# Kernel optimization log

Measured on AMD Instinct MI355X. Metric: run time of the kernel, lower is better.

Reference implementation:

```python
import jax, jax.numpy as jnp
import numpy as np

N = 20000   # nodes
E = 160000  # edges
IN = 16     # in_channels
H = 32      # hidden_channels
MID = 32    # edge-MLP hidden width


def setup_inputs() -> dict:
    key = jax.random.key(0)
    ks = jax.random.split(key, 18)
    s = 0.1  # param scale
    return {
        "x": jax.random.normal(ks[0], (N, IN), jnp.float32),
        "edge_index": jax.random.randint(ks[1], (2, E), 0, N, dtype=jnp.int64),
        "edge_weight": jax.random.uniform(ks[2], (E,), jnp.float32),
        # edge_net1: Linear(1,32) -> SiLU -> Linear(32, IN*H)
        "en1_w1": jax.random.normal(ks[3], (1, MID), jnp.float32) * s,
        "en1_b1": jax.random.normal(ks[4], (MID,), jnp.float32) * s,
        "en1_w2": jax.random.normal(ks[5], (MID, IN * H), jnp.float32) * s,
        "en1_b2": jax.random.normal(ks[6], (IN * H,), jnp.float32) * s,
        "root1": jax.random.normal(ks[7], (IN, H), jnp.float32) * s,
        "bias1": jax.random.normal(ks[8], (H,), jnp.float32) * s,
        # edge_net2: Linear(1,32) -> SiLU -> Linear(32, H*H)
        "en2_w1": jax.random.normal(ks[9], (1, MID), jnp.float32) * s,
        "en2_b1": jax.random.normal(ks[10], (MID,), jnp.float32) * s,
        "en2_w2": jax.random.normal(ks[11], (MID, H * H), jnp.float32) * s,
        "en2_b2": jax.random.normal(ks[12], (H * H,), jnp.float32) * s,
        "root2": jax.random.normal(ks[13], (H, H), jnp.float32) * s,
        "bias2": jax.random.normal(ks[14], (H,), jnp.float32) * s,
        "dec_w": jax.random.normal(ks[15], (H, 1), jnp.float32) * s,
        "dec_b": jax.random.normal(ks[16], (1,), jnp.float32) * s,
    }


def _nnconv(x, src, dst, inv_cnt, e, w1, b1, w2, b2, root, bias, cin, cout):
    # edge MLP -> per-edge [cin, cout] weight matrix
    h = jax.nn.silu(e @ w1 + b1)            # [E, MID]
    w = (h @ w2 + b2).reshape(-1, cin, cout)  # [E, cin, cout]
    msg = jnp.einsum('ei,eio->eo', x[src], w)  # per-edge matmul [E, cout]
    agg = jax.ops.segment_sum(msg, dst, num_segments=N) * inv_cnt  # scatter-mean
    return agg + x @ root + bias


def reference(x, edge_index, edge_weight,
              en1_w1, en1_b1, en1_w2, en1_b2, root1, bias1,
              en2_w1, en2_b1, en2_w2, en2_b2, root2, bias2,
              dec_w, dec_b):
    src, dst = edge_index[0], edge_index[1]
    e = edge_weight[:, None]  # [E, 1]
    cnt = jax.ops.segment_sum(jnp.ones((E,), x.dtype), dst, num_segments=N)
    inv_cnt = (1.0 / jnp.maximum(cnt, 1.0))[:, None]  # [N, 1]
    h = _nnconv(x, src, dst, inv_cnt, e, en1_w1, en1_b1, en1_w2, en1_b2, root1, bias1, IN, H)
    h = jax.nn.silu(h)
    h = _nnconv(h, src, dst, inv_cnt, e, en2_w1, en2_b1, en2_w2, en2_b2, root2, bias2, H, H)
    h = jax.nn.silu(h)
    out = h @ dec_w + dec_b  # [N, 1]
    return out[:, 0]
```

## Files before the change

kernel.cpp:

```cpp
#include <hip/hip_runtime.h>
#include <hip/hip_bf16.h>

#define NN 20000
#define EE 160000
#define HH 32
#define MIDD 32
#define NB 64
#define EPB 2500

typedef _Float16 f16x4 __attribute__((ext_vector_type(4)));
typedef _Float16 f16x8 __attribute__((ext_vector_type(8)));
typedef float f32x4 __attribute__((ext_vector_type(4)));

__device__ __forceinline__ float silu_f(float v) {
    return __fdividef(v, 1.0f + __expf(-v));
}

__device__ __forceinline__ void gload_lds_b32(const void* gsrc, void* ldst) {
    __builtin_amdgcn_global_load_lds(
        (const __attribute__((address_space(1))) void*)gsrc,
        (__attribute__((address_space(3))) void*)ldst, 4, 0, 0);
}

__device__ __forceinline__ int swz4(int e) { return ((e >> 2) & 3) << 2; }

__global__ __launch_bounds__(256) void prep_kernel(
    const int* __restrict__ ei,
    const float* __restrict__ w2a, const float* __restrict__ b2a,
    const float* __restrict__ ra,
    const float* __restrict__ w2b, const float* __restrict__ b2b,
    const float* __restrict__ rb,
    const float* __restrict__ x,
    unsigned int* __restrict__ histG,
    _Float16* __restrict__ Wt1, _Float16* __restrict__ Wt2,
    _Float16* __restrict__ x16, int* __restrict__ flag) {
    const int t = threadIdx.x;
    if (blockIdx.x < NB) {
        __shared__ unsigned int h2[NN / 2];
        for (int i = t; i < NN / 2; i += 256) h2[i] = 0u;
        __syncthreads();
        const int base = blockIdx.x * EPB;
        for (int e = base + t; e < base + EPB; e += 256) {
            int d = ei[EE + e];
            atomicAdd(&h2[d >> 1], 1u << ((d & 1) * 16));
        }
        __syncthreads();
        unsigned int* outp = histG + (size_t)blockIdx.x * NN;
        for (int n = t; n < NN; n += 256)
            outp[n] = (h2[n >> 1] >> ((n & 1) * 16)) & 0xFFFFu;
        return;
    }
    if (blockIdx.x == NB && t == 0) *flag = 0;
    int idx = (blockIdx.x - NB) * 256 + t;
    if (idx < 17408) {
        int o = idx / 544, k = idx % 544;
        float v;
        if (k < 512) {
            int m = k & 31, i = k >> 5;
            v = w2a[m * 512 + i * 32 + o];
        } else if (k < 528) {
            v = b2a[(k - 512) * 32 + o];
        } else {
            v = ra[(k - 528) * 32 + o];
        }
        Wt1[o * 544 + k] = (_Float16)v;
    } else if (idx < 52224) {
        int j = idx - 17408;
        int o = j / 1088, k = j % 1088;
        float v;
        if (k < 1024) {
            int m = k & 31, i = k >> 5;
            v = w2b[m * 1024 + i * 32 + o];
        } else if (k < 1056) {
            v = b2b[(k - 1024) * 32 + o];
        } else {
            v = rb[(k - 1056) * 32 + o];
        }
        Wt2[o * 1088 + k] = (_Float16)v;
    } else if (idx < 52224 + NN * 16) {
        int j = idx - 52224;
        x16[j] = (_Float16)x[j];
    }
}

__global__ __launch_bounds__(256) void colscan_scan_kernel(
    unsigned int* __restrict__ histG, int* __restrict__ cnt,
    float* __restrict__ invc, int* __restrict__ off, int* __restrict__ flag) {
    const int n = blockIdx.x * 256 + threadIdx.x;
    if (n < NN) {
        unsigned int s = 0;
        #pragma unroll 4
        for (int b = 0; b < NB; ++b) {
            unsigned int v = histG[(size_t)b * NN + n];
            histG[(size_t)b * NN + n] = s;
            s += v;
        }
        cnt[n] = (int)s;
        invc[n] = 1.0f / fmaxf((float)s, 1.0f);
    }
    __threadfence();
    __shared__ int isLast;
    __shared__ int wtot[4];
    if (threadIdx.x == 0)
        isLast = (atomicAdd(flag, 1) == (int)gridDim.x - 1) ? 1 : 0;
    __syncthreads();
    if (!isLast) return;

    const int t = threadIdx.x;
    const int base = t * 80;
    int s = 0;
    if (base + 80 <= NN) {
        #pragma unroll
        for (int q = 0; q < 20; ++q) {
            int4 v = ((const int4*)(cnt + base))[q];
            s += v.x + v.y + v.z + v.w;
        }
    }
    const int lane = t & 63, wv = t >> 6;
    int incl = s;
    #pragma unroll
    for (int d2 = 1; d2 < 64; d2 <<= 1) {
        int u = __shfl_up(incl, d2);
        if (lane >= d2) incl += u;
    }
    if (lane == 63) wtot[wv] = incl;
    __syncthreads();
    int wbase = 0;
    for (int p2 = 0; p2 < wv; ++p2) wbase += wtot[p2];
    int running = wbase + incl - s;
    if (base + 80 <= NN) {
        #pragma unroll
        for (int q = 0; q < 20; ++q) {
            int4 v = ((const int4*)(cnt + base))[q];
            int4 o;
            o.x = running;
            o.y = running + v.x;
            o.z = o.y + v.y;
            o.w = o.z + v.z;
            ((int4*)(off + base))[q] = o;
            running = o.w + v.w;
        }
    }
    if (t == 0) off[NN] = EE;
}

__global__ __launch_bounds__(256) void scatter2_kernel(
    const int* __restrict__ ei, const float* __restrict__ ewt,
    const int* __restrict__ off, const unsigned int* __restrict__ histG,
    int2* __restrict__ spair) {
    __shared__ unsigned int r2[NN / 2];
    const int t = threadIdx.x, b = blockIdx.x;
    for (int i = t; i < NN / 2; i += 256) r2[i] = 0u;
    __syncthreads();
    const int base = b * EPB;
    const unsigned int* hb = histG + (size_t)b * NN;
    for (int e = base + t; e < base + EPB; e += 256) {
        int d = ei[EE + e];
        unsigned int old = atomicAdd(&r2[d >> 1], 1u << ((d & 1) * 16));
        int rank = (int)((old >> ((d & 1) * 16)) & 0xFFFFu);
        int pos = off[d] + (int)hb[d] + rank;
        spair[pos] = make_int2(ei[e], __float_as_int(ewt[e]));
    }
}


template <int CIN, bool DECODE>
__global__ __launch_bounds__(512, 4) void fused_layer(
    const _Float16* __restrict__ xin16, const int* __restrict__ spair,
    const int* __restrict__ off, const float* __restrict__ invc,
    const float* __restrict__ w1, const float* __restrict__ b1,
    const _Float16* __restrict__ Wt, const float* __restrict__ bias,
    void* __restrict__ outp, const float* __restrict__ dw,
    const float* __restrict__ db) {
    constexpr int K = 34 * CIN;
    constexpr int LDK = K + 4;
    constexpr int steps = K / 32;
    constexpr int CAP = 192;
    constexpr int RPG = 128 / CIN;
    constexpr int LPR = CIN / 2;
    constexpr int NIH = CIN / 16;

    extern __shared__ char smem[];
    _Float16* Fl = (_Float16*)smem;
    char* poolb = smem + (size_t)16 * LDK * 2;
    int* Ps = (int*)poolb;
    _Float16* Xs = (_Float16*)(poolb + (2 * CAP + 64) * 4);
    _Float16* Hs = Xs + CAP * CIN;
    float* red = (float*)poolb;

    const int t = threadIdx.x;
    const int n0 = blockIdx.x * 16;
    const int lane = t & 63, w = t >> 6;
    const int col = lane & 15, g4 = (lane >> 4) * 4;
    const int qcl = col & 1, qhi = col >> 1;

    const int E0 = off[n0], E1 = off[n0 + 16];
    const int L = E1 - E0;

    const int d0 = n0 + w * 2;
    const int e0l0 = off[d0] - E0;
    const int e1l0 = off[d0 + 1] - E0;
    const int e1l1 = off[d0 + 2] - E0;

    const float w1v = w1[t & 31];
    const float b1v = b1[t & 31];

    f32x4 aS[2][2][NIH];
    f32x4 a0[2][NIH];
    #pragma unroll
    for (int c = 0; c < 2; ++c) {
        #pragma unroll
        for (int mh = 0; mh < 2; ++mh)
            #pragma unroll
            for (int ih = 0; ih < NIH; ++ih) aS[c][mh][ih] = (f32x4){0.f, 0.f, 0.f, 0.f};
        #pragma unroll
        for (int ih = 0; ih < NIH; ++ih) a0[c][ih] = (f32x4){0.f, 0.f, 0.f, 0.f};
    }

    for (int base = 0; base < L; base += CAP) {
        const int Lc = (L - base < CAP) ? (L - base) : CAP;

        for (int c = w * 64; c < 2 * Lc; c += 512) {
            int gidx = 2 * (E0 + base) + c + lane;
            gidx = (gidx < 2 * EE) ? gidx : (2 * EE - 1);
            gload_lds_b32(spair + gidx, Ps + c);
        }
        __syncthreads();

        {
            const int G = (Lc + RPG - 1) / RPG;
            const int er = lane / LPR, ecp = lane % LPR;
            for (int p = w; p < G; p += 8) {
                int el = p * RPG + er; el = (el < Lc - 1) ? el : (Lc - 1);
                int sn = Ps[2 * el];
                int sp = (CIN == 32) ? (ecp ^ swz4(el)) : ecp;
                gload_lds_b32(xin16 + (size_t)sn * CIN + 2 * sp,
                              Xs + (size_t)p * RPG * CIN);
            }
        }
        for (int idx = t; idx < Lc * 32; idx += 512) {
            int e = idx >> 5, m = idx & 31;
            float ew = __int_as_float(Ps[2 * e + 1]);
            int slot = (((m >> 1) ^ swz4(e)) << 1) + (m & 1);
            Hs[e * 32 + slot] = (_Float16)silu_f(fmaf(ew, w1v, b1v));
        }
        __syncthreads();

        #pragma unroll
        for (int c = 0; c < 2; ++c) {
            int lo = ((c == 0) ? e0l0 : e1l0) - base;
            int hi = ((c == 0) ? e1l0 : e1l1) - base;
            lo = (lo < 0) ? 0 : lo;
            hi = (hi > Lc) ? Lc : hi;
            for (int ks = lo; ks < hi; ks += 32) {
                f16x8 bf[NIH];
                #pragma unroll
                for (int ih = 0; ih < NIH; ++ih) {
                    const int qx = ih * 8 + qhi;
                    #pragma unroll
                    for (int j = 0; j < 4; ++j) {
                        int k1 = ks + g4 + j, k2 = k1 + 16;
                        int c1 = (k1 < hi) ? k1 : (Lc - 1);
                        int c2 = (k2 < hi) ? k2 : (Lc - 1);
                        if (CIN == 32) {
                            bf[ih][j]     = Xs[c1 * 32 + ((qx ^ swz4(c1)) << 1) + qcl];
                            bf[ih][j + 4] = Xs[c2 * 32 + ((qx ^ swz4(c2)) << 1) + qcl];
                        } else {
                            bf[ih][j]     = Xs[c1 * CIN + ih * 16 + col];
                            bf[ih][j + 4] = Xs[c2 * CIN + ih * 16 + col];
                        }
                    }
                }
                f16x8 af[2];
                #pragma unroll
                for (int mh = 0; mh < 2; ++mh) {
                    const int qh = mh * 8 + qhi;
                    #pragma unroll
                    for (int j = 0; j < 4; ++j) {
                        int k1 = ks + g4 + j, k2 = k1 + 16;
                        int c1 = (k1 < hi) ? k1 : (Lc - 1);
                        int c2 = (k2 < hi) ? k2 : (Lc - 1);
                        _Float16 v1 = Hs[c1 * 32 + ((qh ^ swz4(c1)) << 1) + qcl];
                        _Float16 v2 = Hs[c2 * 32 + ((qh ^ swz4(c2)) << 1) + qcl];
                        af[mh][j]     = (k1 < hi) ? v1 : (_Float16)0;
                        af[mh][j + 4] = (k2 < hi) ? v2 : (_Float16)0;
                    }
                }
                f16x8 ao;
                #pragma unroll
                for (int j = 0; j < 4; ++j) {
                    int k1 = ks + g4 + j, k2 = k1 + 16;
                    ao[j]     = (col == 0 && k1 < hi) ? (_Float16)1 : (_Float16)0;
                    ao[j + 4] = (col == 0 && k2 < hi) ? (_Float16)1 : (_Float16)0;
                }
                #pragma unroll
                for (int mh = 0; mh < 2; ++mh)
                    #pragma unroll
                    for (int ih = 0; ih < NIH; ++ih)
                        aS[c][mh][ih] = __builtin_amdgcn_mfma_f32_16x16x32_f16(
                            af[mh], bf[ih], aS[c][mh][ih], 0, 0, 0);
                #pragma unroll
                for (int ih = 0; ih < NIH; ++ih)
                    a0[c][ih] = __builtin_amdgcn_mfma_f32_16x16x32_f16(
                        ao, bf[ih], a0[c][ih], 0, 0, 0);
            }
        }
        if (base + CAP < L) __syncthreads();
    }

    #pragma unroll
    for (int c = 0; c < 2; ++c) {
        const int d = n0 + w * 2 + c;
        const float iv = invc[d];
        _Float16* Fr = Fl + (size_t)(w * 2 + c) * LDK;
        #pragma unroll
        for (int mh = 0; mh < 2; ++mh)
            #pragma unroll
            for (int ih = 0; ih < NIH; ++ih)
                #pragma unroll
                for (int r = 0; r < 4; ++r)
                    Fr[32 * (ih * 16 + col) + mh * 16 + g4 + r] =
                        (_Float16)(aS[c][mh][ih][r] * iv);
        if (g4 == 0) {
            #pragma unroll
            for (int ih = 0; ih < NIH; ++ih)
                Fr[32 * CIN + ih * 16 + col] = (_Float16)(a0[c][ih][0] * iv);
        }
        if (lane >= CIN && lane < 2 * CIN)
            Fr[32 * CIN + lane] = xin16[(size_t)d * CIN + (lane - CIN)];
    }
    __syncthreads();

    const int o16 = col, g = lane >> 4;

    const _Float16* Arow = Fl + (size_t)o16 * LDK + g * 4;
    const _Float16* B0 = Wt + (size_t)o16 * K + g * 4;
    const _Float16* B1 = Wt + (size_t)(o16 + 16) * K + g * 4;

    f32x4 acc0 = {0.f, 0.f, 0.f, 0.f};
    f32x4 acc1 = {0.f, 0.f, 0.f, 0.f};

    const int sb = (steps * w) >> 3;
    const int se = (steps * (w + 1)) >> 3;
    #pragma unroll 2
    for (int s = sb; s < se; ++s) {
        const int k0 = s * 32;
        f16x4 alo = *(const f16x4*)(Arow + k0);
        f16x4 ahi = *(const f16x4*)(Arow + k0 + 16);
        f16x4 b0l = *(const f16x4*)(B0 + k0);
        f16x4 b0h = *(const f16x4*)(B0 + k0 + 16);
        f16x4 b1l = *(const f16x4*)(B1 + k0);
        f16x4 b1h = *(const f16x4*)(B1 + k0 + 16);
        f16x8 a, bb0, bb1;
        #pragma unroll
        for (int j = 0; j < 4; ++j) {
            a[j] = alo[j];  a[j + 4] = ahi[j];
            bb0[j] = b0l[j]; bb0[j + 4] = b0h[j];
            bb1[j] = b1l[j]; bb1[j + 4] = b1h[j];
        }
        acc0 = __builtin_amdgcn_mfma_f32_16x16x32_f16(a, bb0, acc0, 0, 0, 0);
        acc1 = __builtin_amdgcn_mfma_f32_16x16x32_f16(a, bb1, acc1, 0, 0, 0);
    }

    if (w > 0) {
        float* rw = red + (w - 1) * 512;
        #pragma unroll
        for (int r = 0; r < 4; ++r) {
            rw[(g * 4 + r) * 32 + o16]      = acc0[r];
            rw[(g * 4 + r) * 32 + 16 + o16] = acc1[r];
        }
    }
    __syncthreads();
    if (w == 0) {
        #pragma unroll
        for (int r = 0; r < 4; ++r) {
            const int ro = (g * 4 + r) * 32 + o16;
            #pragma unroll
            for (int p = 0; p < 7; ++p) {
                acc0[r] += red[p * 512 + ro];
                acc1[r] += red[p * 512 + ro + 16];
            }
        }
        const float bb0 = bias[o16], bb1 = bias[o16 + 16];
        const int nrow = n0 + g * 4;
        if (!DECODE) {
            _Float16* op = (_Float16*)outp;
            #pragma unroll
            for (int r = 0; r < 4; ++r) {
                op[(size_t)(nrow + r) * 32 + o16]      = (_Float16)silu_f(acc0[r] + bb0);
                op[(size_t)(nrow + r) * 32 + 16 + o16] = (_Float16)silu_f(acc1[r] + bb1);
            }
        } else {
            float* op = (float*)outp;
            const float w0 = dw[o16], w1vv = dw[o16 + 16];
            const float dbv = db[0];
            #pragma unroll
            for (int r = 0; r < 4; ++r) {
                float p = silu_f(acc0[r] + bb0) * w0 + silu_f(acc1[r] + bb1) * w1vv;
                p += __shfl_xor(p, 1);
                p += __shfl_xor(p, 2);
                p += __shfl_xor(p, 4);
                p += __shfl_xor(p, 8);
                if (o16 == 0) op[nrow + r] = p + dbv;
            }
        }
    }
}


extern "C" void kernel_launch(void* const* d_in, const int* in_sizes, int n_in,
                              void* d_out, int out_size, void* d_ws, size_t ws_size,
                              hipStream_t stream) {
    const float* x      = (const float*)d_in[0];
    const int*   ei     = (const int*)d_in[1];
    const float* ew     = (const float*)d_in[2];
    const float* en1_w1 = (const float*)d_in[3];
    const float* en1_b1 = (const float*)d_in[4];
    const float* en1_w2 = (const float*)d_in[5];
    const float* en1_b2 = (const float*)d_in[6];
    const float* root1  = (const float*)d_in[7];
    const float* bias1  = (const float*)d_in[8];
    const float* en2_w1 = (const float*)d_in[9];
    const float* en2_b1 = (const float*)d_in[10];
    const float* en2_w2 = (const float*)d_in[11];
    const float* en2_b2 = (const float*)d_in[12];
    const float* root2  = (const float*)d_in[13];
    const float* bias2  = (const float*)d_in[14];
    const float* dec_w  = (const float*)d_in[15];
    const float* dec_b  = (const float*)d_in[16];
    float* out = (float*)d_out;
    (void)in_sizes; (void)n_in; (void)out_size; (void)ws_size;

    char* wp = (char*)d_ws;
    auto alloc = [&](size_t bytes) {
        char* p = wp;
        wp += (bytes + 255) & ~(size_t)255;
        return p;
    };
    unsigned int* histG = (unsigned int*)alloc((size_t)NB * NN * 4);
    int*      cnt   = (int*)alloc((size_t)NN * 4);
    int*      off   = (int*)alloc((size_t)(NN + 1) * 4);
    float*    invc  = (float*)alloc((size_t)NN * 4);
    int2*     spair = (int2*)alloc((size_t)EE * 8);
    _Float16* h1h   = (_Float16*)alloc((size_t)NN * 32 * 2);
    _Float16* x16   = (_Float16*)alloc((size_t)NN * 16 * 2);
    _Float16* Wt1   = (_Float16*)alloc((size_t)17408 * 2);
    _Float16* Wt2   = (_Float16*)alloc((size_t)34816 * 2);
    int*      flag  = (int*)alloc(256);

    const int build_blocks = (52224 + NN * 16 + 255) / 256;
    prep_kernel<<<NB + build_blocks, 256, 0, stream>>>(
        ei, en1_w2, en1_b2, root1, en2_w2, en2_b2, root2, x,
        histG, Wt1, Wt2, x16, flag);
    colscan_scan_kernel<<<(NN + 255) / 256, 256, 0, stream>>>(
        histG, cnt, invc, off, flag);
    scatter2_kernel<<<NB, 256, 0, stream>>>(ei, ew, off, histG, spair);

    auto f1 = fused_layer<16, false>;
    auto f2 = fused_layer<32, true>;
    (void)hipFuncSetAttribute((const void*)f1,
                              hipFuncAttributeMaxDynamicSharedMemorySize, 163840);
    (void)hipFuncSetAttribute((const void*)f2,
                              hipFuncAttributeMaxDynamicSharedMemorySize, 163840);

    const size_t lds1 = (size_t)16 * (34 * 16 + 4) * 2 + (448 * 4 + 192 * 16 * 2 + 192 * 64);
    const size_t lds2 = (size_t)16 * (34 * 32 + 4) * 2 + (448 * 4 + 192 * 32 * 2 + 192 * 64);

    fused_layer<16, false><<<NN / 16, 512, lds1, stream>>>(
        x16, (const int*)spair, off, invc, en1_w1, en1_b1, Wt1, bias1, h1h,
        nullptr, nullptr);
    fused_layer<32, true><<<NN / 16, 512, lds2, stream>>>(
        h1h, (const int*)spair, off, invc, en2_w1, en2_b1, Wt2, bias2, out,
        dec_w, dec_b);
}
```

Baseline: 104.7 us.

## Drop LDS XOR swizzle, pad edge tiles, and double prep histogram blocks

Removes the XOR swizzle on the gathered X and H tiles in LDS and uses plain row-major indexing. The tiles get padding rows, and the gather loads 32 extra clamped rows, so the MFMA operand loads no longer need per-element index clamping and the address arithmetic gets simpler. Separately, the histogram/scatter stage now uses 128 blocks with half as many edges each instead of 64. Without the swizzle, the column-strided LDS reads may hit more bank conflicts, and the padded buffers raise LDS use per block.

```diff
diff --git a/kernel.cpp b/kernel.cpp
--- a/kernel.cpp
+++ b/kernel.cpp
@@ -5,8 +5,8 @@
 #define EE 160000
 #define HH 32
 #define MIDD 32
-#define NB 64
-#define EPB 2500
+#define NB 128
+#define EPB 1250
 
 typedef _Float16 f16x4 __attribute__((ext_vector_type(4)));
 typedef _Float16 f16x8 __attribute__((ext_vector_type(8)));
@@ -21,8 +21,6 @@
         (const __attribute__((address_space(1))) void*)gsrc,
         (__attribute__((address_space(3))) void*)ldst, 4, 0, 0);
 }
-
-__device__ __forceinline__ int swz4(int e) { return ((e >> 2) & 3) << 2; }
 
 __global__ __launch_bounds__(256) void prep_kernel(
     const int* __restrict__ ei,
@@ -179,20 +177,21 @@
     constexpr int RPG = 128 / CIN;
     constexpr int LPR = CIN / 2;
     constexpr int NIH = CIN / 16;
+    constexpr int XROWS = CAP + 40;
+    constexpr int HROWS = CAP + 32;
 
     extern __shared__ char smem[];
     _Float16* Fl = (_Float16*)smem;
     char* poolb = smem + (size_t)16 * LDK * 2;
     int* Ps = (int*)poolb;
     _Float16* Xs = (_Float16*)(poolb + (2 * CAP + 64) * 4);
-    _Float16* Hs = Xs + CAP * CIN;
+    _Float16* Hs = Xs + XROWS * CIN;
     float* red = (float*)poolb;
 
     const int t = threadIdx.x;
     const int n0 = blockIdx.x * 16;
     const int lane = t & 63, w = t >> 6;
     const int col = lane & 15, g4 = (lane >> 4) * 4;
-    const int qcl = col & 1, qhi = col >> 1;
 
     const int E0 = off[n0], E1 = off[n0 + 16];
     const int L = E1 - E0;
@@ -227,22 +226,20 @@
         }
         __syncthreads();
 
-        {
-            const int G = (Lc + RPG - 1) / RPG;
+        if (Lc > 0) {
+            const int G = (Lc + 32 + RPG - 1) / RPG;
             const int er = lane / LPR, ecp = lane % LPR;
             for (int p = w; p < G; p += 8) {
                 int el = p * RPG + er; el = (el < Lc - 1) ? el : (Lc - 1);
                 int sn = Ps[2 * el];
-                int sp = (CIN == 32) ? (ecp ^ swz4(el)) : ecp;
-                gload_lds_b32(xin16 + (size_t)sn * CIN + 2 * sp,
+                gload_lds_b32(xin16 + (size_t)sn * CIN + 2 * ecp,
                               Xs + (size_t)p * RPG * CIN);
             }
         }
         for (int idx = t; idx < Lc * 32; idx += 512) {
-            int e = idx >> 5, m = idx & 31;
+            int e = idx >> 5;
             float ew = __int_as_float(Ps[2 * e + 1]);
-            int slot = (((m >> 1) ^ swz4(e)) << 1) + (m & 1);
-            Hs[e * 32 + slot] = (_Float16)silu_f(fmaf(ew, w1v, b1v));
+            Hs[idx] = (_Float16)silu_f(fmaf(ew, w1v, b1v));
         }
         __syncthreads();
 
@@ -253,43 +250,30 @@
             lo = (lo < 0) ? 0 : lo;
             hi = (hi > Lc) ? Lc : hi;
             for (int ks = lo; ks < hi; ks += 32) {
+                const int k1b = ks + g4;
                 f16x8 bf[NIH];
                 #pragma unroll
-                for (int ih = 0; ih < NIH; ++ih) {
-                    const int qx = ih * 8 + qhi;
+                for (int ih = 0; ih < NIH; ++ih)
                     #pragma unroll
                     for (int j = 0; j < 4; ++j) {
-                        int k1 = ks + g4 + j, k2 = k1 + 16;
-                        int c1 = (k1 < hi) ? k1 : (Lc - 1);
-                        int c2 = (k2 < hi) ? k2 : (Lc - 1);
-                        if (CIN == 32) {
-                            bf[ih][j]     = Xs[c1 * 32 + ((qx ^ swz4(c1)) << 1) + qcl];
-                            bf[ih][j + 4] = Xs[c2 * 32 + ((qx ^ swz4(c2)) << 1) + qcl];
-                        } else {
-                            bf[ih][j]     = Xs[c1 * CIN + ih * 16 + col];
-                            bf[ih][j + 4] = Xs[c2 * CIN + ih * 16 + col];
-                        }
+                        bf[ih][j]     = Xs[(k1b + j) * CIN + ih * 16 + col];
+                        bf[ih][j + 4] = Xs[(k1b + j + 16) * CIN + ih * 16 + col];
                     }
-                }
                 f16x8 af[2];
                 #pragma unroll
-                for (int mh = 0; mh < 2; ++mh) {
-                    const int qh = mh * 8 + qhi;
+                for (int mh = 0; mh < 2; ++mh)
                     #pragma unroll
                     for (int j = 0; j < 4; ++j) {
-                        int k1 = ks + g4 + j, k2 = k1 + 16;
-                        int c1 = (k1 < hi) ? k1 : (Lc - 1);
-                        int c2 = (k2 < hi) ? k2 : (Lc - 1);
-                        _Float16 v1 = Hs[c1 * 32 + ((qh ^ swz4(c1)) << 1) + qcl];
-                        _Float16 v2 = Hs[c2 * 32 + ((qh ^ swz4(c2)) << 1) + qcl];
+                        int k1 = k1b + j, k2 = k1 + 16;
+                        _Float16 v1 = Hs[k1 * 32 + mh * 16 + col];
+                        _Float16 v2 = Hs[k2 * 32 + mh * 16 + col];
                         af[mh][j]     = (k1 < hi) ? v1 : (_Float16)0;
                         af[mh][j + 4] = (k2 < hi) ? v2 : (_Float16)0;
                     }
-                }
                 f16x8 ao;
                 #pragma unroll
                 for (int j = 0; j < 4; ++j) {
-                    int k1 = ks + g4 + j, k2 = k1 + 16;
+                    int k1 = k1b + j, k2 = k1 + 16;
                     ao[j]     = (col == 0 && k1 < hi) ? (_Float16)1 : (_Float16)0;
                     ao[j + 4] = (col == 0 && k2 < hi) ? (_Float16)1 : (_Float16)0;
                 }
@@ -463,8 +447,10 @@
     (void)hipFuncSetAttribute((const void*)f2,
                               hipFuncAttributeMaxDynamicSharedMemorySize, 163840);
 
-    const size_t lds1 = (size_t)16 * (34 * 16 + 4) * 2 + (448 * 4 + 192 * 16 * 2 + 192 * 64);
-    const size_t lds2 = (size_t)16 * (34 * 32 + 4) * 2 + (448 * 4 + 192 * 32 * 2 + 192 * 64);
+    const size_t lds1 = (size_t)16 * (34 * 16 + 4) * 2 + 448 * 4
+                      + (size_t)(192 + 40) * 16 * 2 + (size_t)(192 + 32) * 32 * 2;
+    const size_t lds2 = (size_t)16 * (34 * 32 + 4) * 2 + 448 * 4
+                      + (size_t)(192 + 40) * 32 * 2 + (size_t)(192 + 32) * 32 * 2;
 
     fused_layer<16, false><<<NN / 16, 512, lds1, stream>>>(
         x16, (const int*)spair, off, invc, en1_w1, en1_b1, Wt1, bias1, h1h,
```

Result: no change. 106.2 us (+1.4%).
